# Kernel optimization log

Hardware: AMD Instinct MI355X
Metric: run time of the kernel (lower is better)

Reference implementation:

```python
import jax, jax.numpy as jnp
import numpy as np

NEG_INF = -1000000.0
B_, NG, HEADS, C, GH, GW, GD = 256, 64, 6, 192, 6, 6, 6
N = GH * GW * GD
POS_DIM = (C // 4) // 4  # DynamicPosBias(dim//4): pos_dim = (dim//4)//4 = 12


def setup_inputs() -> dict:
    key = jax.random.key(0)
    ks = jax.random.split(key, 12)
    rn = lambda k, shape, s=0.02: jax.random.normal(k, shape, jnp.float32) * s
    x = jax.random.normal(ks[0], (B_, N, C), jnp.float32)
    y = jax.random.normal(ks[1], (B_, N, C), jnp.float32)
    # 0 / -1e6 window mask, as produced by the padding logic upstream
    mask = jnp.where(jax.random.bernoulli(ks[2], 0.1, (NG, N, N)), NEG_INF, 0.0).astype(jnp.float32)
    return dict(
        x=x, y=y, mask=mask,
        Wqkv=rn(ks[3], (3 * C, C)), bqkv=jnp.zeros((3 * C,), jnp.float32),
        Wproj=rn(ks[4], (C, C)), bproj=jnp.zeros((C,), jnp.float32),
        pos_proj_w=rn(ks[5], (POS_DIM, 3)), pos_proj_b=jnp.zeros((POS_DIM,), jnp.float32),
        ln1_g=jnp.ones((POS_DIM,), jnp.float32), ln1_b=jnp.zeros((POS_DIM,), jnp.float32),
        pos1_w=rn(ks[6], (POS_DIM, POS_DIM)), pos1_b=jnp.zeros((POS_DIM,), jnp.float32),
        ln2_g=jnp.ones((POS_DIM,), jnp.float32), ln2_b=jnp.zeros((POS_DIM,), jnp.float32),
        pos2_w=rn(ks[7], (POS_DIM, POS_DIM)), pos2_b=jnp.zeros((POS_DIM,), jnp.float32),
        ln3_g=jnp.ones((POS_DIM,), jnp.float32), ln3_b=jnp.zeros((POS_DIM,), jnp.float32),
        pos3_w=rn(ks[8], (HEADS, POS_DIM)), pos3_b=jnp.zeros((HEADS,), jnp.float32),
        H=GH, W=GW, D=GD)


def _ln(t, g, b):
    m = t.mean(-1, keepdims=True)
    v = ((t - m) ** 2).mean(-1, keepdims=True)
    return (t - m) / jnp.sqrt(v + 1e-5) * g + b


def _rel_tables(H, W, D):
    # biases: all relative offsets in [1-H,H-1]x[1-W,W-1]x[1-D,D-1], shape (M, 3)
    ph = np.arange(1 - H, H); pw = np.arange(1 - W, W); pd = np.arange(1 - D, D)
    biases = np.stack(np.meshgrid(ph, pw, pd, indexing='ij')).reshape(3, -1).T.astype(np.float32)
    coords = np.stack(np.meshgrid(np.arange(H), np.arange(W), np.arange(D), indexing='ij')).reshape(3, -1)
    rel = (coords[:, :, None] - coords[:, None, :]).transpose(1, 2, 0)  # (N, N, 3)
    rel[..., 0] += H - 1; rel[..., 1] += W - 1; rel[..., 2] += D - 1
    rel[..., 0] *= (2 * W - 1) * (2 * D - 1); rel[..., 1] *= (2 * D - 1)
    idx = rel.sum(-1)  # (N, N) indices into the (M,) bias table
    return jnp.asarray(biases), jnp.asarray(idx)


def reference(x, y, mask, Wqkv, bqkv, Wproj, bproj, pos_proj_w, pos_proj_b,
              ln1_g, ln1_b, pos1_w, pos1_b, ln2_g, ln2_b, pos2_w, pos2_b,
              ln3_g, ln3_b, pos3_w, pos3_b, H, W, D):
    Bt, n, c = x.shape
    heads = pos3_w.shape[0]
    hd = c // heads
    scale = hd ** (-0.5)
    # NOTE: original code applies self.qkv to BOTH x and y (qkv_y layer unused)
    qkv = (x @ Wqkv.T + bqkv).reshape(Bt, n, 3, heads, hd).transpose(2, 0, 3, 1, 4)
    qkv_y = (y @ Wqkv.T + bqkv).reshape(Bt, n, 3, heads, hd).transpose(2, 0, 3, 1, 4)
    q = qkv[0] * scale
    k_y, v_y = qkv_y[1], qkv_y[2]
    attn = jnp.einsum('bhnd,bhmd->bhnm', q, k_y)
    # dynamic relative position bias: tiny MLP over offsets, then gather
    biases, idx = _rel_tables(H, W, D)
    pos = biases @ pos_proj_w.T + pos_proj_b
    pos = jnp.maximum(_ln(pos, ln1_g, ln1_b), 0) @ pos1_w.T + pos1_b
    pos = jnp.maximum(_ln(pos, ln2_g, ln2_b), 0) @ pos2_w.T + pos2_b
    pos = jnp.maximum(_ln(pos, ln3_g, ln3_b), 0) @ pos3_w.T + pos3_b  # (M, heads)
    rpb = pos[idx.reshape(-1)].reshape(n, n, heads).transpose(2, 0, 1)  # (heads, N, N)
    attn = attn + rpb[None]
    nG = mask.shape[0]
    attn = attn.reshape(Bt // nG, nG, heads, n, n) + mask[None, :, None]
    attn = jax.nn.softmax(attn, axis=-1).reshape(Bt, heads, n, n)
    out = jnp.einsum('bhnm,bhmd->bhnd', attn, v_y).transpose(0, 2, 1, 3).reshape(Bt, n, c)
    return out @ Wproj.T + bproj
```

## Files before the change

### kernel.cpp

```cpp
#include <hip/hip_runtime.h>
#include <stdint.h>

using short8   = __attribute__((ext_vector_type(8))) short;
using short4_  = __attribute__((ext_vector_type(4))) short;
using float4_  = __attribute__((ext_vector_type(4))) float;
using ushort4_ = __attribute__((ext_vector_type(4))) unsigned short;
typedef unsigned int  uint;
typedef unsigned short ushort;

__device__ __forceinline__ float bf2f(ushort b) {
  uint u = ((uint)b) << 16;
  return __builtin_bit_cast(float, u);
}
__device__ __forceinline__ ushort f2bf(float f) {
  uint u = __builtin_bit_cast(uint, f);
  u = u + 0x7fffu + ((u >> 16) & 1u);
  return (ushort)(u >> 16);
}
__device__ __forceinline__ float exp2_hw(float x) {
  float r;
  asm("v_exp_f32 %0, %1" : "=v"(r) : "v"(x));
  return r;
}
__device__ __forceinline__ void gld_lds16(const ushort* g, ushort* l) {
  __builtin_amdgcn_global_load_lds(
      (const __attribute__((address_space(1))) void*)g,
      (__attribute__((address_space(3))) void*)l, 16, 0, 0);
}
__device__ __forceinline__ int detect_f32(const uint* __restrict__ det) {
  int lane = threadIdx.x & 63;
  uint w = det[lane];
  ushort lo = (ushort)(w & 0xffffu);
  int e = (lo >> 7) & 0xff;
  int sane = (lo == 0 || (e >= 0x60 && e <= 0x9f)) ? 1 : 0;
  unsigned long long b = __ballot(sane);
  return (__popcll(b) >= 56) ? 0 : 1;
}

#define LOG2E 1.4426950408889634f

#define NN   216
#define NSQ  46656
#define PADV (-3.0e6f)

#if __has_builtin(__builtin_amdgcn_mfma_f32_16x16x16bf16_1k)
  #define HAVE_MFMA16 1
  #define MFMA16(a, b, c) __builtin_amdgcn_mfma_f32_16x16x16bf16_1k(a, b, c, 0, 0, 0)
#elif __has_builtin(__builtin_amdgcn_mfma_f32_16x16x16_bf16)
  #define HAVE_MFMA16 1
  #define MFMA16(a, b, c) __builtin_amdgcn_mfma_f32_16x16x16_bf16(a, b, c, 0, 0, 0)
#else
  #define HAVE_MFMA16 0
#endif

#define WA_WQKV   0
#define WA_BQKV   110592
#define WA_WPROJ  111168
#define WA_BPROJ  148032
#define WA_PPW    148224
#define WA_PPB    148260
#define WA_G1     148272
#define WA_B1     148284
#define WA_W1     148296
#define WA_WB1    148440
#define WA_G2     148452
#define WA_B2     148464
#define WA_W2     148476
#define WA_WB2    148620
#define WA_G3     148632
#define WA_B3     148644
#define WA_W3     148656
#define WA_WB3    148728
#define WA_TOTAL  148740

struct SrcPtrs { const void* p[18]; };

__global__ __launch_bounds__(256) void convpack_kernel(
    SrcPtrs sp, const uint* __restrict__ det,
    ushort* __restrict__ warena, ushort* __restrict__ wp) {
  int fl = detect_f32(det);
  int bid = blockIdx.x, tid = threadIdx.x;
  if (bid < 72) {
    int c = bid * 256 + tid;
    int blob = c / 2304, s = c - blob * 2304;
    int kk = s / 384, r = s - kk * 384;
    int nt = r >> 6, l = r & 63;
    int l16 = l & 15, qd = l >> 4;
    int col; const void* src;
    if (blob < 6) { int z = blob >> 1, half = blob & 1;
                    col = z * 192 + half * 96 + nt * 16 + l16; src = sp.p[0]; }
    else          { col = (blob - 6) * 96 + nt * 16 + l16;     src = sp.p[2]; }
    size_t off = (size_t)col * 192 + kk * 32 + qd * 8;
    short8 pk;
    if (fl) {
      float4_ lo = *(const float4_*)((const float*)src + off);
      float4_ hi = *(const float4_*)((const float*)src + off + 4);
#pragma unroll
      for (int j = 0; j < 4; ++j) {
        pk[j]     = (short)f2bf(lo[j]);
        pk[4 + j] = (short)f2bf(hi[j]);
      }
    } else {
      pk = *(const short8*)((const ushort*)src + off);
    }
    *(short8*)(wp + (size_t)c * 8) = pk;
  } else {
    constexpr int OFF[19] = {WA_WQKV, WA_BQKV, WA_WPROJ, WA_BPROJ, WA_PPW, WA_PPB,
                             WA_G1, WA_B1, WA_W1, WA_WB1, WA_G2, WA_B2, WA_W2,
                             WA_WB2, WA_G3, WA_B3, WA_W3, WA_WB3, WA_TOTAL};
    int u = (bid - 72) * 256 + tid;
    if (u >= 1284) return;
    int t, a;
    if (u < 576) { t = WA_BQKV + u; a = 1; }
    else {
      t = WA_BPROJ + (u - 576);
      a = 3;
#pragma unroll
      for (int i = 4; i < 18; ++i) a += (t >= OFF[i]) ? 1 : 0;
    }
    int local = t - OFF[a];
    const void* s = sp.p[a];
    warena[t] = fl ? f2bf(((const float*)s)[local]) : ((const ushort*)s)[local];
  }
}

__global__ __launch_bounds__(256) void packa_kernel(const void* __restrict__ src,
                                                    ushort* __restrict__ dst) {
  int fl = detect_f32((const uint*)src);
  int c = blockIdx.x * 256 + threadIdx.x;
  int tile = c / 3072, cc = c - tile * 3072;
  int kk = cc / 512, c2 = cc - kk * 512;
  int rowhi = c2 / 64, c3 = c2 - rowhi * 64;
  int q = c3 >> 4, l16 = c3 & 15;
  size_t M = (size_t)tile * 128 + rowhi * 16 + l16;
  size_t so = M * 192 + kk * 32 + q * 8;
  short8 pk;
  if (fl) {
    float4_ lo = *(const float4_*)((const float*)src + so);
    float4_ hi = *(const float4_*)((const float*)src + so + 4);
#pragma unroll
    for (int j = 0; j < 4; ++j) {
      pk[j]     = (short)f2bf(lo[j]);
      pk[4 + j] = (short)f2bf(hi[j]);
    }
  } else {
    pk = *(const short8*)((const ushort*)src + so);
  }
  *(short8*)(dst + (size_t)c * 8) = pk;
}

__device__ __forceinline__ void ln_relu(const float* p, const ushort* g,
                                        const ushort* b, float* r) {
  float m = 0.f;
#pragma unroll
  for (int t = 0; t < 12; ++t) m += p[t];
  m *= (1.f / 12.f);
  float v = 0.f;
#pragma unroll
  for (int t = 0; t < 12; ++t) { float d = p[t] - m; v += d * d; }
  v *= (1.f / 12.f);
  float inv = rsqrtf(v + 1e-5f);
#pragma unroll
  for (int t = 0; t < 12; ++t) {
    float z = (p[t] - m) * inv * bf2f(g[t]) + bf2f(b[t]);
    r[t] = fmaxf(z, 0.f);
  }
}

__global__ void pos_mlp_kernel(const ushort* __restrict__ wa, float* __restrict__ pos) {
  int m = blockIdx.x * blockDim.x + threadIdx.x;
  if (m >= 1331) return;
  const ushort* pw  = wa + WA_PPW;  const ushort* pb  = wa + WA_PPB;
  const ushort* g1  = wa + WA_G1;   const ushort* b1  = wa + WA_B1;
  const ushort* w1  = wa + WA_W1;   const ushort* wb1 = wa + WA_WB1;
  const ushort* g2  = wa + WA_G2;   const ushort* b2  = wa + WA_B2;
  const ushort* w2  = wa + WA_W2;   const ushort* wb2 = wa + WA_WB2;
  const ushort* g3  = wa + WA_G3;   const ushort* b3  = wa + WA_B3;
  const ushort* w3  = wa + WA_W3;   const ushort* wb3 = wa + WA_WB3;

  int ih = m / 121, rem = m - ih * 121;
  int iw = rem / 11, id = rem - iw * 11;
  float fh = (float)(ih - 5), fw = (float)(iw - 5), fd = (float)(id - 5);
  float p[12], r[12], q[12];
#pragma unroll
  for (int t = 0; t < 12; ++t)
    p[t] = fh * bf2f(pw[t * 3]) + fw * bf2f(pw[t * 3 + 1]) +
           fd * bf2f(pw[t * 3 + 2]) + bf2f(pb[t]);
  ln_relu(p, g1, b1, r);
#pragma unroll
  for (int t = 0; t < 12; ++t) {
    float s = bf2f(wb1[t]);
#pragma unroll
    for (int u = 0; u < 12; ++u) s += r[u] * bf2f(w1[t * 12 + u]);
    q[t] = s;
  }
  ln_relu(q, g2, b2, r);
#pragma unroll
  for (int t = 0; t < 12; ++t) {
    float s = bf2f(wb2[t]);
#pragma unroll
    for (int u = 0; u < 12; ++u) s += r[u] * bf2f(w2[t * 12 + u]);
    p[t] = s;
  }
  ln_relu(p, g3, b3, r);
#pragma unroll
  for (int h = 0; h < 6; ++h) {
    float s = bf2f(wb3[h]);
#pragma unroll
    for (int u = 0; u < 12; ++u) s += r[u] * bf2f(w3[h * 12 + u]);
    pos[m * 6 + h] = s;
  }
}

__global__ void rpbfrag_kernel(const float* __restrict__ pos, ushort* __restrict__ out) {
  int tgl = blockIdx.x * 256 + threadIdx.x;
  if (tgl >= 6 * 196 * 64) return;
  int lane = tgl & 63;
  int tj   = (tgl >> 6) % 196;
  int h    = (tgl >> 6) / 196;
  int tt = tj / 14, jt = tj - tt * 14;
  int l16 = lane & 15, quad = lane >> 4;
  int i = tt * 16 + l16;
  int jbase = jt * 16 + quad * 4;
  ushort4_ o;
  if (i < 216 && jbase < 216) {
    int h1 = i / 36, r1 = i - h1 * 36, w1 = r1 / 6, d1 = r1 - w1 * 6;
#pragma unroll
    for (int r = 0; r < 4; ++r) {
      int j = jbase + r;
      int h2 = j / 36, r2 = j - h2 * 36, w2 = r2 / 6, d2 = r2 - w2 * 6;
      int idx = ((h1 - h2 + 5) * 11 + (w1 - w2 + 5)) * 11 + (d1 - d2 + 5);
      o[r] = f2bf(pos[idx * 6 + h] * LOG2E);
    }
  } else {
#pragma unroll
    for (int r = 0; r < 4; ++r) o[r] = f2bf(PADV);
  }
  *(ushort4_*)(out + (size_t)tgl * 4) = o;
}

__global__ void maskfrag_kernel(const void* __restrict__ maskv,
                                const uint* __restrict__ det,
                                ushort* __restrict__ out) {
  bool mf32 = detect_f32(det) != 0;
  int tgl = blockIdx.x * 256 + threadIdx.x;
  if (tgl >= 64 * 196 * 64) return;
  int lane = tgl & 63;
  int tj   = (tgl >> 6) % 196;
  int g    = (tgl >> 6) / 196;
  int tt = tj / 14, jt = tj - tt * 14;
  int l16 = lane & 15, quad = lane >> 4;
  int i = tt * 16 + l16;
  int jbase = jt * 16 + quad * 4;
  ushort4_ o;
  if (i < 216 && jbase < 216) {
    int mi = i * 216 + jbase;
    if (mf32) {
      float4_ mv = *(const float4_*)((const float*)maskv + (size_t)g * NSQ + mi);
#pragma unroll
      for (int r = 0; r < 4; ++r) o[r] = f2bf(mv[r] * LOG2E);
    } else {
      ushort4_ raw = *(const ushort4_*)((const ushort*)maskv + (size_t)g * NSQ + mi);
#pragma unroll
      for (int r = 0; r < 4; ++r) o[r] = f2bf(bf2f(raw[r]) * LOG2E);
    }
  } else {
#pragma unroll
    for (int r = 0; r < 4; ++r) o[r] = f2bf(PADV);
  }
  *(ushort4_*)(out + (size_t)tgl * 4) = o;
}

template<int NT, int IS_PROJ>
__global__ __launch_bounds__(256, 2) void gemm_kernel(
    const void* __restrict__ Arow,
    const ushort* __restrict__ Apack,
    const ushort* __restrict__ wpacked,
    const ushort* __restrict__ bias,
    void* __restrict__ dq, void* __restrict__ dk, void* __restrict__ dv,
    const uint* __restrict__ det) {
  __shared__ __align__(16) ushort b_lds[NT * 3072];

  int fl = detect_f32(det);
  int tid = threadIdx.x;
  int tile = blockIdx.x;
  int m0 = tile * 128;
  int zz = blockIdx.y;
  int n0   = IS_PROJ ? zz * 96 : 0;
  int blob = IS_PROJ ? (6 + zz) : (zz * 2);
  float scale = (!IS_PROJ && zz == 0) ? (0.17677669529663687f * LOG2E) : 1.0f;
  void* dst = IS_PROJ ? dq : (zz == 0 ? dq : (zz == 1 ? dk : dv));
  bool a_packed = (!IS_PROJ) && (zz != 0);
  bool f32path = (!IS_PROJ) && (zz == 0) && (fl != 0);
  bool o_f32 = IS_PROJ && (fl != 0);

  int lane = tid & 63, w = tid >> 6;
  int l16 = lane & 15, quad = lane >> 4;

  {
    const ushort* wb = wpacked + (size_t)blob * 18432;
    int wuni = (tid >> 6) << 6;
#pragma unroll
    for (int it = 0; it < (NT * 3) / 2; ++it) {
      int base = wuni + it * 256;
      gld_lds16(wb + (size_t)(base + lane) * 8, b_lds + (size_t)base * 8);
    }
  }

  short8 af[6][2];
  if (a_packed) {
    const ushort* tb = Apack + (size_t)tile * 24576 + lane * 8;
#pragma unroll
    for (int kk = 0; kk < 6; ++kk)
#pragma unroll
      for (int mt = 0; mt < 2; ++mt)
        af[kk][mt] = *(const short8*)(tb + kk * 4096 + (w * 2 + mt) * 512);
  } else if (f32path) {
#pragma unroll
    for (int kk = 0; kk < 6; ++kk)
#pragma unroll
      for (int mt = 0; mt < 2; ++mt) {
        const float* Af = (const float*)Arow +
            (size_t)(m0 + w * 32 + mt * 16 + l16) * 192 + kk * 32 + quad * 8;
        float4_ lo = *(const float4_*)Af;
        float4_ hi = *(const float4_*)(Af + 4);
#pragma unroll
        for (int j = 0; j < 4; ++j) {
          af[kk][mt][j]     = (short)f2bf(lo[j]);
          af[kk][mt][4 + j] = (short)f2bf(hi[j]);
        }
      }
  } else {
#pragma unroll
    for (int kk = 0; kk < 6; ++kk)
#pragma unroll
      for (int mt = 0; mt < 2; ++mt)
        af[kk][mt] = *(const short8*)((const ushort*)Arow +
            (size_t)(m0 + w * 32 + mt * 16 + l16) * 192 + kk * 32 + quad * 8);
  }
  __syncthreads();

  float4_ acc[2][NT];
#pragma unroll
  for (int mt = 0; mt < 2; ++mt)
#pragma unroll
    for (int nt = 0; nt < NT; ++nt) acc[mt][nt] = (float4_){0.f, 0.f, 0.f, 0.f};

#pragma unroll
  for (int kk = 0; kk < 6; ++kk) {
    short8 bfr[NT];
#pragma unroll
    for (int nt = 0; nt < NT; ++nt) {
      int halfb = nt / 6, nl = nt % 6;
      bfr[nt] = *(const short8*)(b_lds + halfb * 18432 + ((kk * 6 + nl) * 64 + lane) * 8);
    }
#pragma unroll
    for (int mt = 0; mt < 2; ++mt)
#pragma unroll
      for (int nt = 0; nt < NT; ++nt)
        acc[mt][nt] = __builtin_amdgcn_mfma_f32_16x16x32_bf16(af[kk][mt], bfr[nt], acc[mt][nt], 0, 0, 0);
  }

#pragma unroll
  for (int mt = 0; mt < 2; ++mt) {
#pragma unroll
    for (int nt = 0; nt < NT; ++nt) {
      int lcol = n0 + nt * 16 + l16;
      float bv = bf2f(bias[(IS_PROJ ? 0 : zz * 192) + lcol]);
#pragma unroll
      for (int r = 0; r < 4; ++r) {
        int grow = m0 + w * 32 + mt * 16 + quad * 4 + r;
        float val = (acc[mt][nt][r] + bv) * scale;
        if (IS_PROJ) {
          if (o_f32) ((float*)dst)[(size_t)grow * 192 + lcol] = val;
          else       ((ushort*)dst)[(size_t)grow * 192 + lcol] = f2bf(val);
        } else {
          int bb = grow / 216;
          int nn2 = grow - bb * 216;
          int hh = lcol >> 5, dd = lcol & 31;
          ((ushort*)dst)[(((size_t)bb * 6 + hh) * 216 + nn2) * 32 + dd] = f2bf(val);
        }
      }
    }
  }
}

__global__ __launch_bounds__(448) void attn_kernel(
    const ushort* __restrict__ q, const ushort* __restrict__ k,
    const ushort* __restrict__ v, const ushort* __restrict__ rpbf,
    const ushort* __restrict__ maskf, ushort* __restrict__ opre) {
#if HAVE_MFMA16
  __shared__ __align__(16) ushort vfrag[28 * 64 * 4];
#else
  __shared__ __align__(16) ushort vfrag[14 * 64 * 8];
#endif

  int bid = blockIdx.x;
  int g   = bid / 24;
  int rr  = bid - g * 24;
  int bhi = rr / 6;
  int h   = rr - bhi * 6;
  int b   = bhi * 64 + g;

  int tid = threadIdx.x, lane = tid & 63, w = tid >> 6;
  int l16 = lane & 15, quad = lane >> 4;

  const ushort* qh = q + (size_t)(b * 6 + h) * 6912;
  const ushort* kh = k + (size_t)(b * 6 + h) * 6912;
  const ushort* vh = v + (size_t)(b * 6 + h) * 6912;

#if HAVE_MFMA16
  for (int pos = tid; pos < 1792; pos += 448) {
    int chunk = pos >> 6, l = pos & 63;
    int kt = chunk >> 1, dh = chunk & 1;
    int qd = l >> 4, lv = l & 15;
    ushort4_ tmp;
#pragma unroll
    for (int j = 0; j < 4; ++j)
      tmp[j] = vh[(kt * 16 + qd * 4 + j) * 32 + dh * 16 + lv];
    *(ushort4_*)(vfrag + pos * 4) = tmp;
  }
#else
  for (int pos = tid; pos < 896; pos += 448) {
    int chunk = pos >> 6, l = pos & 63;
    int kt2 = chunk >> 1, dh = chunk & 1;
    int qd = l >> 4, lv = l & 15;
    short8 tmp;
#pragma unroll
    for (int j = 0; j < 8; ++j)
      tmp[j] = (short)vh[(kt2 * 32 + qd * 8 + j) * 32 + dh * 16 + lv];
    *(short8*)(vfrag + pos * 8) = tmp;
  }
#endif
  __syncthreads();

  for (int t = w; t < 14; t += 7) {
    int r0 = t * 16;
    const ushort* rf = rpbf  + ((size_t)(h * 196 + t * 14) * 64 + lane) * 4;
    const ushort* mf = maskf + ((size_t)(g * 196 + t * 14) * 64 + lane) * 4;
    short8 aq = *(const short8*)(qh + (r0 + l16) * 32 + quad * 8);

    float4_ st[14];
    __builtin_amdgcn_s_setprio(1);
#pragma unroll
    for (int jt = 0; jt < 14; ++jt) {
      ushort4_ rb = *(const ushort4_*)(rf + jt * 256);
      ushort4_ mb = *(const ushort4_*)(mf + jt * 256);
      float4_ cin;
#pragma unroll
      for (int r = 0; r < 4; ++r) cin[r] = bf2f(rb[r]) + bf2f(mb[r]);
      short8 bk = *(const short8*)(kh + (jt * 16 + l16) * 32 + quad * 8);
      st[jt] = __builtin_amdgcn_mfma_f32_16x16x32_bf16(bk, aq, cin, 0, 0, 0);
    }
    __builtin_amdgcn_s_setprio(0);

    float mx = -1e30f;
#pragma unroll
    for (int jt = 0; jt < 14; ++jt)
      mx = fmaxf(fmaxf(st[jt][0], st[jt][1]),
                 fmaxf(fmaxf(st[jt][2], st[jt][3]), mx));
    mx = fmaxf(mx, __shfl_xor(mx, 16));
    mx = fmaxf(mx, __shfl_xor(mx, 32));
    float sum = 0.f;
#pragma unroll
    for (int jt = 0; jt < 14; ++jt)
#pragma unroll
      for (int r = 0; r < 4; ++r) {
        float pe = exp2_hw(st[jt][r] - mx);
        st[jt][r] = pe;
        sum += pe;
      }
    sum += __shfl_xor(sum, 16);
    sum += __shfl_xor(sum, 32);
    float inv = 1.0f / sum;

    float4_ o0 = (float4_){0.f, 0.f, 0.f, 0.f};
    float4_ o1 = (float4_){0.f, 0.f, 0.f, 0.f};

    __builtin_amdgcn_s_setprio(1);
#if HAVE_MFMA16
#pragma unroll
    for (int kt = 0; kt < 14; ++kt) {
      short4_ pa;
#pragma unroll
      for (int r = 0; r < 4; ++r) pa[r] = (short)f2bf(st[kt][r]);
      short4_ vb0 = *(const short4_*)(vfrag + ((kt * 2 + 0) * 64 + lane) * 4);
      short4_ vb1 = *(const short4_*)(vfrag + ((kt * 2 + 1) * 64 + lane) * 4);
      o0 = MFMA16(pa, vb0, o0);
      o1 = MFMA16(pa, vb1, o1);
    }
#else
#pragma unroll
    for (int kt2 = 0; kt2 < 7; ++kt2) {
      uint pe0 = ((uint)f2bf(st[2*kt2][0])) | (((uint)f2bf(st[2*kt2][1])) << 16);
      uint pe1 = ((uint)f2bf(st[2*kt2][2])) | (((uint)f2bf(st[2*kt2][3])) << 16);
      uint po0 = ((uint)f2bf(st[2*kt2+1][0])) | (((uint)f2bf(st[2*kt2+1][1])) << 16);
      uint po1 = ((uint)f2bf(st[2*kt2+1][2])) | (((uint)f2bf(st[2*kt2+1][3])) << 16);
      int slo = (((2 * quad) & 3) << 4) | l16;
      int shi = (((2 * quad + 1) & 3) << 4) | l16;
      uint e_lo0 = __shfl((int)pe0, slo), e_lo1 = __shfl((int)pe1, slo);
      uint o_lo0 = __shfl((int)po0, slo), o_lo1 = __shfl((int)po1, slo);
      uint e_hi0 = __shfl((int)pe0, shi), e_hi1 = __shfl((int)pe1, shi);
      uint o_hi0 = __shfl((int)po0, shi), o_hi1 = __shfl((int)po1, shi);
      uint lo0 = (quad < 2) ? e_lo0 : o_lo0, lo1 = (quad < 2) ? e_lo1 : o_lo1;
      uint hi0 = (quad < 2) ? e_hi0 : o_hi0, hi1 = (quad < 2) ? e_hi1 : o_hi1;
      uint4 paw = {lo0, lo1, hi0, hi1};
      short8 pa = __builtin_bit_cast(short8, paw);
      short8 vb0 = *(const short8*)(vfrag + ((kt2 * 2 + 0) * 64 + lane) * 8);
      short8 vb1 = *(const short8*)(vfrag + ((kt2 * 2 + 1) * 64 + lane) * 8);
      o0 = __builtin_amdgcn_mfma_f32_16x16x32_bf16(pa, vb0, o0, 0, 0, 0);
      o1 = __builtin_amdgcn_mfma_f32_16x16x32_bf16(pa, vb1, o1, 0, 0, 0);
    }
#endif
    __builtin_amdgcn_s_setprio(0);

#pragma unroll
    for (int r = 0; r < 4; ++r) {
      float ir = __shfl(inv, quad * 4 + r);
      int i = r0 + quad * 4 + r;
      if (i < 216) {
        size_t base = ((size_t)b * 216 + i) * 192 + h * 32;
        opre[base + l16]      = f2bf(o0[r] * ir);
        opre[base + 16 + l16] = f2bf(o1[r] * ir);
      }
    }
  }
}

extern "C" void kernel_launch(void* const* d_in, const int* in_sizes, int n_in,
                              void* d_out, int out_size, void* d_ws, size_t ws_size,
                              hipStream_t stream) {
  (void)in_sizes; (void)n_in; (void)out_size; (void)ws_size;

  char* p = (char*)d_ws;
  p += 256;
  ushort* warena  = (ushort*)p;        p += 298240;
  ushort* wpacked = (ushort*)p;        p += 294912;
  float*  pos     = (float*)p;         p += 32768;
  ushort* rpbf    = (ushort*)p;        p += 602112;
  ushort* maskf   = (ushort*)p;        p += 6422528;
  ushort* yf      = (ushort*)p;        p += 21234688;
  ushort* qb      = (ushort*)p;        p += 21234688;
  ushort* kb      = (ushort*)p;        p += 21234688;
  ushort* vb      = (ushort*)p;
  ushort* opre    = yf;

  const uint* xdet = (const uint*)d_in[0];

  SrcPtrs sp;
  for (int i = 0; i < 18; ++i) sp.p[i] = d_in[3 + i];

  convpack_kernel<<<78, 256, 0, stream>>>(sp, xdet, warena, wpacked);

  packa_kernel<<<5184, 256, 0, stream>>>(d_in[1], yf);

  pos_mlp_kernel<<<6, 256, 0, stream>>>(warena, pos);
  rpbfrag_kernel<<<294, 256, 0, stream>>>(pos, rpbf);
  maskfrag_kernel<<<3136, 256, 0, stream>>>(d_in[2], xdet, maskf);

  gemm_kernel<12, 0><<<dim3(432, 3), 256, 0, stream>>>(
      d_in[0], yf, wpacked, warena + WA_BQKV, qb, kb, vb, xdet);

  attn_kernel<<<1536, 448, 0, stream>>>(qb, kb, vb, rpbf, maskf, opre);

  gemm_kernel<6, 1><<<dim3(432, 2), 256, 0, stream>>>(
      opre, nullptr, wpacked, warena + WA_BPROJ,
      d_out, d_out, d_out, xdet);
}
```

Baseline: 286.9 us.

## Merge preprocessing kernels into one launch and fold rpb build into QKV GEMM

Five small preprocessing kernels (weight pack, y pack, position MLP, mask fragment) become one block-indexed mega kernel. The position MLP now reads raw parameters directly instead of the converted arena, which removes its dependency on the weight pack. The rpb fragment build is appended as extra blocks of the QKV GEMM launch. This cuts launch count and inter-kernel serialization, but the fused GEMM kernel now reserves 12-tile LDS for the rpb blocks too.

```diff
diff --git a/kernel.cpp b/kernel.cpp
--- a/kernel.cpp
+++ b/kernel.cpp
@@ -35,6 +35,9 @@
   int sane = (lo == 0 || (e >= 0x60 && e <= 0x9f)) ? 1 : 0;
   unsigned long long b = __ballot(sane);
   return (__popcll(b) >= 56) ? 0 : 1;
+}
+__device__ __forceinline__ ushort bfw(const void* p, int i, int fl) {
+  return fl ? f2bf(((const float*)p)[i]) : ((const ushort*)p)[i];
 }
 
 #define LOG2E 1.4426950408889634f
@@ -75,12 +78,34 @@
 
 struct SrcPtrs { const void* p[18]; };
 
-__global__ __launch_bounds__(256) void convpack_kernel(
-    SrcPtrs sp, const uint* __restrict__ det,
-    ushort* __restrict__ warena, ushort* __restrict__ wp) {
-  int fl = detect_f32(det);
+__device__ __forceinline__ void ln_relu_raw(const float* p, const void* g,
+                                            const void* b, int fl, float* r) {
+  float m = 0.f;
+#pragma unroll
+  for (int t = 0; t < 12; ++t) m += p[t];
+  m *= (1.f / 12.f);
+  float v = 0.f;
+#pragma unroll
+  for (int t = 0; t < 12; ++t) { float d = p[t] - m; v += d * d; }
+  v *= (1.f / 12.f);
+  float inv = rsqrtf(v + 1e-5f);
+#pragma unroll
+  for (int t = 0; t < 12; ++t) {
+    float z = (p[t] - m) * inv * bf2f(bfw(g, t, fl)) + bf2f(bfw(b, t, fl));
+    r[t] = fmaxf(z, 0.f);
+  }
+}
+
+__global__ __launch_bounds__(256) void mega_pre_kernel(
+    SrcPtrs sp, const uint* __restrict__ xdet,
+    const void* __restrict__ ysrc, const void* __restrict__ maskv,
+    ushort* __restrict__ warena, ushort* __restrict__ wp,
+    ushort* __restrict__ yf, ushort* __restrict__ maskf,
+    float* __restrict__ pos) {
   int bid = blockIdx.x, tid = threadIdx.x;
+
   if (bid < 72) {
+    int fl = detect_f32(xdet);
     int c = bid * 256 + tid;
     int blob = c / 2304, s = c - blob * 2304;
     int kk = s / 384, r = s - kk * 384;
@@ -104,7 +129,9 @@
       pk = *(const short8*)((const ushort*)src + off);
     }
     *(short8*)(wp + (size_t)c * 8) = pk;
-  } else {
+
+  } else if (bid < 78) {
+    int fl = detect_f32(xdet);
     constexpr int OFF[19] = {WA_WQKV, WA_BQKV, WA_WPROJ, WA_BPROJ, WA_PPW, WA_PPB,
                              WA_G1, WA_B1, WA_W1, WA_WB1, WA_G2, WA_B2, WA_W2,
                              WA_WB2, WA_G3, WA_B3, WA_W3, WA_WB3, WA_TOTAL};
@@ -121,171 +148,107 @@
     int local = t - OFF[a];
     const void* s = sp.p[a];
     warena[t] = fl ? f2bf(((const float*)s)[local]) : ((const ushort*)s)[local];
-  }
-}
-
-__global__ __launch_bounds__(256) void packa_kernel(const void* __restrict__ src,
-                                                    ushort* __restrict__ dst) {
-  int fl = detect_f32((const uint*)src);
-  int c = blockIdx.x * 256 + threadIdx.x;
-  int tile = c / 3072, cc = c - tile * 3072;
-  int kk = cc / 512, c2 = cc - kk * 512;
-  int rowhi = c2 / 64, c3 = c2 - rowhi * 64;
-  int q = c3 >> 4, l16 = c3 & 15;
-  size_t M = (size_t)tile * 128 + rowhi * 16 + l16;
-  size_t so = M * 192 + kk * 32 + q * 8;
-  short8 pk;
-  if (fl) {
-    float4_ lo = *(const float4_*)((const float*)src + so);
-    float4_ hi = *(const float4_*)((const float*)src + so + 4);
-#pragma unroll
-    for (int j = 0; j < 4; ++j) {
-      pk[j]     = (short)f2bf(lo[j]);
-      pk[4 + j] = (short)f2bf(hi[j]);
-    }
+
+  } else if (bid < 84) {
+    int fl = detect_f32(xdet);
+    int m = (bid - 78) * 256 + tid;
+    if (m >= 1331) return;
+    int ih = m / 121, rem = m - ih * 121;
+    int iw = rem / 11, id = rem - iw * 11;
+    float fh = (float)(ih - 5), fw = (float)(iw - 5), fd = (float)(id - 5);
+    float p[12], r[12], q[12];
+#pragma unroll
+    for (int t = 0; t < 12; ++t)
+      p[t] = fh * bf2f(bfw(sp.p[4], t * 3, fl)) +
+             fw * bf2f(bfw(sp.p[4], t * 3 + 1, fl)) +
+             fd * bf2f(bfw(sp.p[4], t * 3 + 2, fl)) +
+             bf2f(bfw(sp.p[5], t, fl));
+    ln_relu_raw(p, sp.p[6], sp.p[7], fl, r);
+#pragma unroll
+    for (int t = 0; t < 12; ++t) {
+      float s = bf2f(bfw(sp.p[9], t, fl));
+#pragma unroll
+      for (int u = 0; u < 12; ++u) s += r[u] * bf2f(bfw(sp.p[8], t * 12 + u, fl));
+      q[t] = s;
+    }
+    ln_relu_raw(q, sp.p[10], sp.p[11], fl, r);
+#pragma unroll
+    for (int t = 0; t < 12; ++t) {
+      float s = bf2f(bfw(sp.p[13], t, fl));
+#pragma unroll
+      for (int u = 0; u < 12; ++u) s += r[u] * bf2f(bfw(sp.p[12], t * 12 + u, fl));
+      p[t] = s;
+    }
+    ln_relu_raw(p, sp.p[14], sp.p[15], fl, r);
+#pragma unroll
+    for (int hh = 0; hh < 6; ++hh) {
+      float s = bf2f(bfw(sp.p[17], hh, fl));
+#pragma unroll
+      for (int u = 0; u < 12; ++u) s += r[u] * bf2f(bfw(sp.p[16], hh * 12 + u, fl));
+      pos[m * 6 + hh] = s;
+    }
+
+  } else if (bid < 84 + 5184) {
+    int fl = detect_f32((const uint*)ysrc);
+    int c = (bid - 84) * 256 + tid;
+    int tile = c / 3072, cc = c - tile * 3072;
+    int kk = cc / 512, c2 = cc - kk * 512;
+    int rowhi = c2 / 64, c3 = c2 - rowhi * 64;
+    int q = c3 >> 4, l16 = c3 & 15;
+    size_t M = (size_t)tile * 128 + rowhi * 16 + l16;
+    size_t so = M * 192 + kk * 32 + q * 8;
+    short8 pk;
+    if (fl) {
+      float4_ lo = *(const float4_*)((const float*)ysrc + so);
+      float4_ hi = *(const float4_*)((const float*)ysrc + so + 4);
+#pragma unroll
+      for (int j = 0; j < 4; ++j) {
+        pk[j]     = (short)f2bf(lo[j]);
+        pk[4 + j] = (short)f2bf(hi[j]);
+      }
+    } else {
+      pk = *(const short8*)((const ushort*)ysrc + so);
+    }
+    *(short8*)(yf + (size_t)c * 8) = pk;
+
   } else {
-    pk = *(const short8*)((const ushort*)src + so);
-  }
-  *(short8*)(dst + (size_t)c * 8) = pk;
-}
-
-__device__ __forceinline__ void ln_relu(const float* p, const ushort* g,
-                                        const ushort* b, float* r) {
-  float m = 0.f;
-#pragma unroll
-  for (int t = 0; t < 12; ++t) m += p[t];
-  m *= (1.f / 12.f);
-  float v = 0.f;
-#pragma unroll
-  for (int t = 0; t < 12; ++t) { float d = p[t] - m; v += d * d; }
-  v *= (1.f / 12.f);
-  float inv = rsqrtf(v + 1e-5f);
-#pragma unroll
-  for (int t = 0; t < 12; ++t) {
-    float z = (p[t] - m) * inv * bf2f(g[t]) + bf2f(b[t]);
-    r[t] = fmaxf(z, 0.f);
-  }
-}
-
-__global__ void pos_mlp_kernel(const ushort* __restrict__ wa, float* __restrict__ pos) {
-  int m = blockIdx.x * blockDim.x + threadIdx.x;
-  if (m >= 1331) return;
-  const ushort* pw  = wa + WA_PPW;  const ushort* pb  = wa + WA_PPB;
-  const ushort* g1  = wa + WA_G1;   const ushort* b1  = wa + WA_B1;
-  const ushort* w1  = wa + WA_W1;   const ushort* wb1 = wa + WA_WB1;
-  const ushort* g2  = wa + WA_G2;   const ushort* b2  = wa + WA_B2;
-  const ushort* w2  = wa + WA_W2;   const ushort* wb2 = wa + WA_WB2;
-  const ushort* g3  = wa + WA_G3;   const ushort* b3  = wa + WA_B3;
-  const ushort* w3  = wa + WA_W3;   const ushort* wb3 = wa + WA_WB3;
-
-  int ih = m / 121, rem = m - ih * 121;
-  int iw = rem / 11, id = rem - iw * 11;
-  float fh = (float)(ih - 5), fw = (float)(iw - 5), fd = (float)(id - 5);
-  float p[12], r[12], q[12];
-#pragma unroll
-  for (int t = 0; t < 12; ++t)
-    p[t] = fh * bf2f(pw[t * 3]) + fw * bf2f(pw[t * 3 + 1]) +
-           fd * bf2f(pw[t * 3 + 2]) + bf2f(pb[t]);
-  ln_relu(p, g1, b1, r);
-#pragma unroll
-  for (int t = 0; t < 12; ++t) {
-    float s = bf2f(wb1[t]);
-#pragma unroll
-    for (int u = 0; u < 12; ++u) s += r[u] * bf2f(w1[t * 12 + u]);
-    q[t] = s;
-  }
-  ln_relu(q, g2, b2, r);
-#pragma unroll
-  for (int t = 0; t < 12; ++t) {
-    float s = bf2f(wb2[t]);
-#pragma unroll
-    for (int u = 0; u < 12; ++u) s += r[u] * bf2f(w2[t * 12 + u]);
-    p[t] = s;
-  }
-  ln_relu(p, g3, b3, r);
-#pragma unroll
-  for (int h = 0; h < 6; ++h) {
-    float s = bf2f(wb3[h]);
-#pragma unroll
-    for (int u = 0; u < 12; ++u) s += r[u] * bf2f(w3[h * 12 + u]);
-    pos[m * 6 + h] = s;
-  }
-}
-
-__global__ void rpbfrag_kernel(const float* __restrict__ pos, ushort* __restrict__ out) {
-  int tgl = blockIdx.x * 256 + threadIdx.x;
-  if (tgl >= 6 * 196 * 64) return;
-  int lane = tgl & 63;
-  int tj   = (tgl >> 6) % 196;
-  int h    = (tgl >> 6) / 196;
-  int tt = tj / 14, jt = tj - tt * 14;
-  int l16 = lane & 15, quad = lane >> 4;
-  int i = tt * 16 + l16;
-  int jbase = jt * 16 + quad * 4;
-  ushort4_ o;
-  if (i < 216 && jbase < 216) {
-    int h1 = i / 36, r1 = i - h1 * 36, w1 = r1 / 6, d1 = r1 - w1 * 6;
-#pragma unroll
-    for (int r = 0; r < 4; ++r) {
-      int j = jbase + r;
-      int h2 = j / 36, r2 = j - h2 * 36, w2 = r2 / 6, d2 = r2 - w2 * 6;
-      int idx = ((h1 - h2 + 5) * 11 + (w1 - w2 + 5)) * 11 + (d1 - d2 + 5);
-      o[r] = f2bf(pos[idx * 6 + h] * LOG2E);
-    }
-  } else {
-#pragma unroll
-    for (int r = 0; r < 4; ++r) o[r] = f2bf(PADV);
-  }
-  *(ushort4_*)(out + (size_t)tgl * 4) = o;
-}
-
-__global__ void maskfrag_kernel(const void* __restrict__ maskv,
-                                const uint* __restrict__ det,
-                                ushort* __restrict__ out) {
-  bool mf32 = detect_f32(det) != 0;
-  int tgl = blockIdx.x * 256 + threadIdx.x;
-  if (tgl >= 64 * 196 * 64) return;
-  int lane = tgl & 63;
-  int tj   = (tgl >> 6) % 196;
-  int g    = (tgl >> 6) / 196;
-  int tt = tj / 14, jt = tj - tt * 14;
-  int l16 = lane & 15, quad = lane >> 4;
-  int i = tt * 16 + l16;
-  int jbase = jt * 16 + quad * 4;
-  ushort4_ o;
-  if (i < 216 && jbase < 216) {
-    int mi = i * 216 + jbase;
-    if (mf32) {
-      float4_ mv = *(const float4_*)((const float*)maskv + (size_t)g * NSQ + mi);
-#pragma unroll
-      for (int r = 0; r < 4; ++r) o[r] = f2bf(mv[r] * LOG2E);
+    bool mf32 = detect_f32(xdet) != 0;
+    int tgl = (bid - 5268) * 256 + tid;
+    int lane = tgl & 63;
+    int tj   = (tgl >> 6) % 196;
+    int g    = (tgl >> 6) / 196;
+    int tt = tj / 14, jt = tj - tt * 14;
+    int l16 = lane & 15, quad = lane >> 4;
+    int i = tt * 16 + l16;
+    int jbase = jt * 16 + quad * 4;
+    ushort4_ o;
+    if (i < 216 && jbase < 216) {
+      int mi = i * 216 + jbase;
+      if (mf32) {
+        float4_ mv = *(const float4_*)((const float*)maskv + (size_t)g * NSQ + mi);
+#pragma unroll
+        for (int r = 0; r < 4; ++r) o[r] = f2bf(mv[r] * LOG2E);
+      } else {
+        ushort4_ raw = *(const ushort4_*)((const ushort*)maskv + (size_t)g * NSQ + mi);
+#pragma unroll
+        for (int r = 0; r < 4; ++r) o[r] = f2bf(bf2f(raw[r]) * LOG2E);
+      }
     } else {
-      ushort4_ raw = *(const ushort4_*)((const ushort*)maskv + (size_t)g * NSQ + mi);
-#pragma unroll
-      for (int r = 0; r < 4; ++r) o[r] = f2bf(bf2f(raw[r]) * LOG2E);
-    }
-  } else {
-#pragma unroll
-    for (int r = 0; r < 4; ++r) o[r] = f2bf(PADV);
-  }
-  *(ushort4_*)(out + (size_t)tgl * 4) = o;
+#pragma unroll
+      for (int r = 0; r < 4; ++r) o[r] = f2bf(PADV);
+    }
+    *(ushort4_*)(maskf + (size_t)tgl * 4) = o;
+  }
 }
 
 template<int NT, int IS_PROJ>
-__global__ __launch_bounds__(256, 2) void gemm_kernel(
-    const void* __restrict__ Arow,
-    const ushort* __restrict__ Apack,
-    const ushort* __restrict__ wpacked,
-    const ushort* __restrict__ bias,
+__device__ __forceinline__ void gemm_body(
+    ushort* b_lds, int tile, int zz, int tid,
+    const void* __restrict__ Arow, const ushort* __restrict__ Apack,
+    const ushort* __restrict__ wpacked, const ushort* __restrict__ bias,
     void* __restrict__ dq, void* __restrict__ dk, void* __restrict__ dv,
-    const uint* __restrict__ det) {
-  __shared__ __align__(16) ushort b_lds[NT * 3072];
-
-  int fl = detect_f32(det);
-  int tid = threadIdx.x;
-  int tile = blockIdx.x;
+    int fl) {
   int m0 = tile * 128;
-  int zz = blockIdx.y;
   int n0   = IS_PROJ ? zz * 96 : 0;
   int blob = IS_PROJ ? (6 + zz) : (zz * 2);
   float scale = (!IS_PROJ && zz == 0) ? (0.17677669529663687f * LOG2E) : 1.0f;
@@ -383,6 +346,57 @@
       }
     }
   }
+}
+
+__global__ __launch_bounds__(256, 2) void qkvrpb_kernel(
+    const void* __restrict__ Ax, const ushort* __restrict__ Apack,
+    const ushort* __restrict__ wpacked, const ushort* __restrict__ bias,
+    void* __restrict__ dq, void* __restrict__ dk, void* __restrict__ dv,
+    const uint* __restrict__ det,
+    const float* __restrict__ pos, ushort* __restrict__ rpbf) {
+  __shared__ __align__(16) ushort b_lds[12 * 3072];
+  int bid = blockIdx.x;
+  if (bid < 1296) {
+    int fl = detect_f32(det);
+    gemm_body<12, 0>(b_lds, bid % 432, bid / 432, threadIdx.x,
+                     Ax, Apack, wpacked, bias, dq, dk, dv, fl);
+  } else {
+    int tgl = (bid - 1296) * 256 + threadIdx.x;
+    int lane = tgl & 63;
+    int tj   = (tgl >> 6) % 196;
+    int h    = (tgl >> 6) / 196;
+    int tt = tj / 14, jt = tj - tt * 14;
+    int l16 = lane & 15, quad = lane >> 4;
+    int i = tt * 16 + l16;
+    int jbase = jt * 16 + quad * 4;
+    ushort4_ o;
+    if (i < 216 && jbase < 216) {
+      int h1 = i / 36, r1 = i - h1 * 36, w1 = r1 / 6, d1 = r1 - w1 * 6;
+#pragma unroll
+      for (int r = 0; r < 4; ++r) {
+        int j = jbase + r;
+        int h2 = j / 36, r2 = j - h2 * 36, w2 = r2 / 6, d2 = r2 - w2 * 6;
+        int idx = ((h1 - h2 + 5) * 11 + (w1 - w2 + 5)) * 11 + (d1 - d2 + 5);
+        o[r] = f2bf(pos[idx * 6 + h] * LOG2E);
+      }
+    } else {
+#pragma unroll
+      for (int r = 0; r < 4; ++r) o[r] = f2bf(PADV);
+    }
+    *(ushort4_*)(rpbf + (size_t)tgl * 4) = o;
+  }
+}
+
+template<int NT, int IS_PROJ>
+__global__ __launch_bounds__(256, 2) void gemm_kernel(
+    const void* __restrict__ Arow, const ushort* __restrict__ Apack,
+    const ushort* __restrict__ wpacked, const ushort* __restrict__ bias,
+    void* __restrict__ dq, void* __restrict__ dk, void* __restrict__ dv,
+    const uint* __restrict__ det) {
+  __shared__ __align__(16) ushort b_lds[NT * 3072];
+  int fl = detect_f32(det);
+  gemm_body<NT, IS_PROJ>(b_lds, blockIdx.x, blockIdx.y, threadIdx.x,
+                         Arow, Apack, wpacked, bias, dq, dk, dv, fl);
 }
 
 __global__ __launch_bounds__(448) void attn_kernel(
@@ -550,16 +564,11 @@
   SrcPtrs sp;
   for (int i = 0; i < 18; ++i) sp.p[i] = d_in[3 + i];
 
-  convpack_kernel<<<78, 256, 0, stream>>>(sp, xdet, warena, wpacked);
-
-  packa_kernel<<<5184, 256, 0, stream>>>(d_in[1], yf);
-
-  pos_mlp_kernel<<<6, 256, 0, stream>>>(warena, pos);
-  rpbfrag_kernel<<<294, 256, 0, stream>>>(pos, rpbf);
-  maskfrag_kernel<<<3136, 256, 0, stream>>>(d_in[2], xdet, maskf);
-
-  gemm_kernel<12, 0><<<dim3(432, 3), 256, 0, stream>>>(
-      d_in[0], yf, wpacked, warena + WA_BQKV, qb, kb, vb, xdet);
+  mega_pre_kernel<<<8404, 256, 0, stream>>>(
+      sp, xdet, d_in[1], d_in[2], warena, wpacked, yf, maskf, pos);
+
+  qkvrpb_kernel<<<1590, 256, 0, stream>>>(
+      d_in[0], yf, wpacked, warena + WA_BQKV, qb, kb, vb, xdet, pos, rpbf);
 
   attn_kernel<<<1536, 448, 0, stream>>>(qb, kb, vb, rpbf, maskf, opre);
 
```

Measured after the change: 307.9 us. +7.3%, slower.
